# Kernel tuning notes

Hardware: AMD Instinct MI355X
Metric: run time of the kernel (lower is better)

## Reference

```python
import jax, jax.numpy as jnp
import numpy as np

EPS = 1e-12  # torch F.normalize eps

N, C, H, W = 64, 512, 40, 40
K = 64  # num_clusters


def setup_inputs() -> dict:
    key = jax.random.key(0)
    k1, k2, k3 = jax.random.split(key, 3)
    x = jax.random.normal(k1, (N, C, H, W), dtype=jnp.float32)
    conv_w = jax.random.normal(k2, (K, C, 1, 1), dtype=jnp.float32) * 0.05
    centroids = jax.random.uniform(k3, (K, C), dtype=jnp.float32)
    return {"x": x, "conv_w": conv_w, "centroids": centroids}


def _l2norm(v, axis):
    return v / jnp.maximum(jnp.sqrt(jnp.sum(v * v, axis=axis, keepdims=True)), EPS)


def reference(x, conv_w, centroids):
    n, c = x.shape[:2]
    k = conv_w.shape[0]
    # descriptor-wise L2 normalization over channels
    xn = _l2norm(x, axis=1)
    xf = xn.reshape(n, c, -1)  # [N, C, P]
    # 1x1 conv (no bias, vladv2=False) == per-pixel matmul with [K, C]
    logits = jnp.einsum('kc,ncp->nkp', conv_w.reshape(k, c), xf)
    a = jax.nn.softmax(logits, axis=1)  # soft assignment over clusters
    # VLAD: sum_p a[n,k,p] * (x[n,:,p] - centroid[k])  (weights are all-ones)
    vlad = jnp.einsum('nkp,ncp->nkc', a, xf) - a.sum(axis=-1)[:, :, None] * centroids[None]
    # intra-normalization over C, flatten, global L2 norm
    vlad = _l2norm(vlad, axis=2).reshape(n, -1)
    vlad = _l2norm(vlad, axis=1)
    return vlad
```

## Files before the change

kernel.cpp:

```cpp
#include <hip/hip_runtime.h>
#include <math.h>

#define EPSF 1e-12f


typedef short bf16x8 __attribute__((ext_vector_type(8)));
typedef float f32x4  __attribute__((ext_vector_type(4)));

__device__ __forceinline__ ushort f2b(float x) {
    unsigned u = __float_as_uint(x);
    return (ushort)((u + 0x7fffu + ((u >> 16) & 1u)) >> 16);
}

__global__ __launch_bounds__(256) void k0_wb(const float* __restrict__ W,
                                             ushort* __restrict__ Wb,
                                             float* __restrict__ asum) {
    int i = blockIdx.x * 256 + threadIdx.x;
    if (i < 64 * 512) Wb[i] = f2b(W[i]);
    if (i < 64 * 64) asum[i] = 0.f;
}

__global__ __launch_bounds__(256) void k2g_gemm1(const float* __restrict__ x,
                                                 const ushort* __restrict__ Wb,
                                                 ushort* __restrict__ a_t,
                                                 float* __restrict__ asum) {
    const int n = blockIdx.y;
    const int p0 = blockIdx.x * 64;
    const int wv = threadIdx.x >> 6, lane = threadIdx.x & 63;
    const int q = lane >> 4, l15 = lane & 15;
    const int pw = p0 + wv * 16;

    const float* xq = x + (size_t)n * 512 * 1600 + (size_t)q * 8 * 1600 + pw + l15;
    const ushort* brow = Wb + l15 * 512 + q * 8;

    f32x4 acc[4] = {};
    float ssp = 0.f;

    float fv[2][8];
    bf16x8 bwv[2][4];
    #pragma unroll
    for (int j = 0; j < 8; j++) fv[0][j] = xq[(size_t)j * 1600];
    #pragma unroll
    for (int nt = 0; nt < 4; nt++) bwv[0][nt] = *(const bf16x8*)(brow + nt * 16 * 512);

    #pragma unroll
    for (int kc = 0; kc < 16; kc++) {
        const int cur = kc & 1, nxt = cur ^ 1;
        if (kc < 15) {
            #pragma unroll
            for (int j = 0; j < 8; j++)
                fv[nxt][j] = xq[(size_t)((kc + 1) * 32 + j) * 1600];
            #pragma unroll
            for (int nt = 0; nt < 4; nt++)
                bwv[nxt][nt] = *(const bf16x8*)(brow + nt * 16 * 512 + (kc + 1) * 32);
        }
        bf16x8 af;
        #pragma unroll
        for (int j = 0; j < 8; j++) {
            float f = fv[cur][j];
            ssp = fmaf(f, f, ssp);
            af[j] = (short)f2b(f);
        }
        #pragma unroll
        for (int nt = 0; nt < 4; nt++)
            acc[nt] = __builtin_amdgcn_mfma_f32_16x16x32_bf16(af, bwv[cur][nt], acc[nt], 0, 0, 0);
    }

    ssp += __shfl_xor(ssp, 16, 64);
    ssp += __shfl_xor(ssp, 32, 64);
    float rn_l = 1.f / fmaxf(sqrtf(ssp), EPSF);
    float rnv[4];
    #pragma unroll
    for (int r = 0; r < 4; r++) rnv[r] = __shfl(rn_l, q * 4 + r, 64);

    float v[4][4];
    float mx[4] = {-3.4e38f, -3.4e38f, -3.4e38f, -3.4e38f};
    #pragma unroll
    for (int nt = 0; nt < 4; nt++)
        #pragma unroll
        for (int r = 0; r < 4; r++) {
            v[nt][r] = acc[nt][r] * rnv[r];
            mx[r] = fmaxf(mx[r], v[nt][r]);
        }
    #pragma unroll
    for (int s = 1; s <= 8; s <<= 1)
        #pragma unroll
        for (int r = 0; r < 4; r++) mx[r] = fmaxf(mx[r], __shfl_xor(mx[r], s, 64));
    float sm[4] = {0.f, 0.f, 0.f, 0.f};
    #pragma unroll
    for (int nt = 0; nt < 4; nt++)
        #pragma unroll
        for (int r = 0; r < 4; r++) { v[nt][r] = __expf(v[nt][r] - mx[r]); sm[r] += v[nt][r]; }
    #pragma unroll
    for (int s = 1; s <= 8; s <<= 1)
        #pragma unroll
        for (int r = 0; r < 4; r++) sm[r] += __shfl_xor(sm[r], s, 64);
    float inv[4];
    #pragma unroll
    for (int r = 0; r < 4; r++) inv[r] = 1.f / sm[r];
    #pragma unroll
    for (int nt = 0; nt < 4; nt++)
        #pragma unroll
        for (int r = 0; r < 4; r++) v[nt][r] *= inv[r];

    #pragma unroll
    for (int nt = 0; nt < 4; nt++) {
        float t = v[nt][0] + v[nt][1] + v[nt][2] + v[nt][3];
        t += __shfl_xor(t, 16, 64);
        t += __shfl_xor(t, 32, 64);
        if (lane < 16) atomicAdd(&asum[n * 64 + nt * 16 + lane], t);
    }

    __shared__ ushort abuf[4][64 * 24];
    #pragma unroll
    for (int nt = 0; nt < 4; nt++)
        #pragma unroll
        for (int r = 0; r < 4; r++)
            abuf[wv][(nt * 16 + l15) * 24 + q * 4 + r] = f2b(v[nt][r] * rnv[r]);
    __syncthreads();
    ushort* dst = a_t + ((size_t)n * 64 + lane) * 1600 + pw;
    const ushort* srcl = &abuf[wv][lane * 24];
    *(uint4*)(dst)     = *(const uint4*)(srcl);
    *(uint4*)(dst + 8) = *(const uint4*)(srcl + 8);
}

__global__ __launch_bounds__(512) void k3_gemm2(const ushort* __restrict__ a_t,
                                                const float* __restrict__ x,
                                                float* __restrict__ out) {
    const int n = blockIdx.y;
    const int c0 = blockIdx.x * 128;
    const int wv = threadIdx.x >> 6, lane = threadIdx.x & 63;
    const int q = lane >> 4, l15 = lane & 15;
    const int cw = c0 + wv * 16;

    const ushort* abase = a_t + ((size_t)n * 64 + l15) * 1600 + q * 8;
    const float*  xbase = x + ((size_t)n * 512 + cw + l15) * 1600 + q * 8;

    f32x4 acc[4] = {};
    #pragma unroll 2
    for (int pc = 0; pc < 1600; pc += 32) {
        bf16x8 af[4];
        #pragma unroll
        for (int mt = 0; mt < 4; mt++)
            af[mt] = *(const bf16x8*)(abase + (size_t)mt * 16 * 1600 + pc);
        const float* xr = xbase + pc;
        float4 f0 = *(const float4*)(xr);
        float4 f1 = *(const float4*)(xr + 4);
        bf16x8 b;
        b[0] = (short)f2b(f0.x); b[1] = (short)f2b(f0.y);
        b[2] = (short)f2b(f0.z); b[3] = (short)f2b(f0.w);
        b[4] = (short)f2b(f1.x); b[5] = (short)f2b(f1.y);
        b[6] = (short)f2b(f1.z); b[7] = (short)f2b(f1.w);
        #pragma unroll
        for (int mt = 0; mt < 4; mt++)
            acc[mt] = __builtin_amdgcn_mfma_f32_16x16x32_bf16(af[mt], b, acc[mt], 0, 0, 0);
    }
    float* ob = out + (size_t)n * 32768 + cw + l15;
    #pragma unroll
    for (int mt = 0; mt < 4; mt++)
        #pragma unroll
        for (int r = 0; r < 4; r++)
            ob[(mt * 16 + q * 4 + r) * 512] = acc[mt][r];
}

__global__ __launch_bounds__(512) void k4ab(const float* __restrict__ vraw,
                                            const float* __restrict__ asum,
                                            const float* __restrict__ cent,
                                            float* __restrict__ rn2,
                                            float* __restrict__ gn) {
    const int n = blockIdx.x;
    const int wv = threadIdx.x >> 6, lane = threadIdx.x & 63;
    __shared__ float rs[64];
    #pragma unroll
    for (int i = 0; i < 8; i++) {
        int k = wv * 8 + i;
        int row = n * 64 + k;
        const float4* vp = (const float4*)(vraw + (size_t)row * 512 + lane * 8);
        const float4* cp = (const float4*)(cent + k * 512 + lane * 8);
        float as = asum[row];
        float4 v0 = vp[0], v1 = vp[1], c0 = cp[0], c1 = cp[1];
        float s = 0.f, t;
        t = v0.x - as * c0.x; s = fmaf(t, t, s);
        t = v0.y - as * c0.y; s = fmaf(t, t, s);
        t = v0.z - as * c0.z; s = fmaf(t, t, s);
        t = v0.w - as * c0.w; s = fmaf(t, t, s);
        t = v1.x - as * c1.x; s = fmaf(t, t, s);
        t = v1.y - as * c1.y; s = fmaf(t, t, s);
        t = v1.z - as * c1.z; s = fmaf(t, t, s);
        t = v1.w - as * c1.w; s = fmaf(t, t, s);
        #pragma unroll
        for (int off = 32; off > 0; off >>= 1) s += __shfl_down(s, off, 64);
        if (lane == 0) { rs[k] = s; rn2[row] = s; }
    }
    __syncthreads();
    if (wv == 0) {
        float t = rs[lane];
        float d = fmaxf(sqrtf(t), EPSF);
        float r = t / (d * d);
        #pragma unroll
        for (int off = 32; off > 0; off >>= 1) r += __shfl_down(r, off, 64);
        if (lane == 0) gn[n] = fmaxf(sqrtf(r), EPSF);
    }
}

__global__ __launch_bounds__(256) void k4c_final(float* __restrict__ vout,
                                                 const float* __restrict__ asum,
                                                 const float* __restrict__ cent,
                                                 const float* __restrict__ rn2,
                                                 const float* __restrict__ gn) {
    int gid = blockIdx.x * 256 + threadIdx.x;
    int idx4 = gid * 4;
    int row = idx4 >> 9;
    int n = row >> 6, k = row & 63, c = idx4 & 511;
    float4 v  = *(const float4*)(vout + idx4);
    float4 cv = *(const float4*)(cent + k * 512 + c);
    float as = asum[row];
    float inv = 1.f / (fmaxf(sqrtf(rn2[row]), EPSF) * gn[n]);
    v.x = (v.x - as * cv.x) * inv;
    v.y = (v.y - as * cv.y) * inv;
    v.z = (v.z - as * cv.z) * inv;
    v.w = (v.w - as * cv.w) * inv;
    *(float4*)(vout + idx4) = v;
}

extern "C" void kernel_launch(void* const* d_in, const int* in_sizes, int n_in,
                              void* d_out, int out_size, void* d_ws, size_t ws_size,
                              hipStream_t stream) {
    const float* x    = (const float*)d_in[0];
    const float* W    = (const float*)d_in[1];
    const float* cent = (const float*)d_in[2];
    float* out = (float*)d_out;
    char* ws = (char*)d_ws;

    ushort* a_t  = (ushort*)(ws + 0);
    ushort* Wb   = (ushort*)(ws + 13107200);
    float*  asum = (float*)(ws + 13172736);
    float*  rn2  = (float*)(ws + 13189120);
    float*  gn   = (float*)(ws + 13205504);

    hipLaunchKernelGGL(k0_wb,     dim3(128),    dim3(256), 0, stream, W, Wb, asum);
    hipLaunchKernelGGL(k2g_gemm1, dim3(25, 64), dim3(256), 0, stream, x, Wb, a_t, asum);
    hipLaunchKernelGGL(k3_gemm2,  dim3(4, 64),  dim3(512), 0, stream, a_t, x, out);
    hipLaunchKernelGGL(k4ab,      dim3(64),     dim3(512), 0, stream, out, asum, cent, rn2, gn);
    hipLaunchKernelGGL(k4c_final, dim3(2048),   dim3(256), 0, stream, out, asum, cent, rn2, gn);
}
```

Before: 400.0 us.

## Fuse both GEMMs and softmax into one kernel with P-split partial sums

The logits GEMM, softmax and VLAD aggregation GEMM now run in one kernel. Each block streams its slice of pixels for one image, converts x to bf16 once, and keeps it in LDS for reuse by the second GEMM. This removes the second full read of x and the round trip of the assignment matrix through global memory. The pixel dimension is split into 5 chunks whose partial VLAD sums are written to workspace. A single finalize kernel then reduces the partials, subtracts the centroid term and applies both normalizations using an LDS stash, replacing two separate kernels. The cost is around 100KB of LDS per block, which limits occupancy, plus a partial-sum buffer that is written and read back by a finalize kernel with only 64 blocks.

```diff
diff --git a/kernel.cpp b/kernel.cpp
--- a/kernel.cpp
+++ b/kernel.cpp
@@ -20,177 +20,189 @@
     if (i < 64 * 64) asum[i] = 0.f;
 }
 
-__global__ __launch_bounds__(256) void k2g_gemm1(const float* __restrict__ x,
-                                                 const ushort* __restrict__ Wb,
-                                                 ushort* __restrict__ a_t,
-                                                 float* __restrict__ asum) {
-    const int n = blockIdx.y;
-    const int p0 = blockIdx.x * 64;
+__global__ __launch_bounds__(512, 2) void kf(const float* __restrict__ x,
+                                             const ushort* __restrict__ Wb,
+                                             float* __restrict__ part,
+                                             float* __restrict__ asum) {
+    const int cb = blockIdx.x;
+    const int n  = blockIdx.y;
     const int wv = threadIdx.x >> 6, lane = threadIdx.x & 63;
     const int q = lane >> 4, l15 = lane & 15;
-    const int pw = p0 + wv * 16;
-
-    const float* xq = x + (size_t)n * 512 * 1600 + (size_t)q * 8 * 1600 + pw + l15;
-    const ushort* brow = Wb + l15 * 512 + q * 8;
-
-    f32x4 acc[4] = {};
-    float ssp = 0.f;
-
-    float fv[2][8];
-    bf16x8 bwv[2][4];
-    #pragma unroll
-    for (int j = 0; j < 8; j++) fv[0][j] = xq[(size_t)j * 1600];
-    #pragma unroll
-    for (int nt = 0; nt < 4; nt++) bwv[0][nt] = *(const bf16x8*)(brow + nt * 16 * 512);
-
-    #pragma unroll
-    for (int kc = 0; kc < 16; kc++) {
-        const int cur = kc & 1, nxt = cur ^ 1;
-        if (kc < 15) {
-            #pragma unroll
-            for (int j = 0; j < 8; j++)
-                fv[nxt][j] = xq[(size_t)((kc + 1) * 32 + j) * 1600];
-            #pragma unroll
-            for (int nt = 0; nt < 4; nt++)
-                bwv[nxt][nt] = *(const bf16x8*)(brow + nt * 16 * 512 + (kc + 1) * 32);
-        }
-        bf16x8 af;
-        #pragma unroll
-        for (int j = 0; j < 8; j++) {
-            float f = fv[cur][j];
-            ssp = fmaf(f, f, ssp);
-            af[j] = (short)f2b(f);
-        }
-        #pragma unroll
-        for (int nt = 0; nt < 4; nt++)
-            acc[nt] = __builtin_amdgcn_mfma_f32_16x16x32_bf16(af, bwv[cur][nt], acc[nt], 0, 0, 0);
-    }
-
-    ssp += __shfl_xor(ssp, 16, 64);
-    ssp += __shfl_xor(ssp, 32, 64);
-    float rn_l = 1.f / fmaxf(sqrtf(ssp), EPSF);
-    float rnv[4];
-    #pragma unroll
-    for (int r = 0; r < 4; r++) rnv[r] = __shfl(rn_l, q * 4 + r, 64);
-
-    float v[4][4];
-    float mx[4] = {-3.4e38f, -3.4e38f, -3.4e38f, -3.4e38f};
-    #pragma unroll
-    for (int nt = 0; nt < 4; nt++)
-        #pragma unroll
-        for (int r = 0; r < 4; r++) {
-            v[nt][r] = acc[nt][r] * rnv[r];
-            mx[r] = fmaxf(mx[r], v[nt][r]);
-        }
-    #pragma unroll
-    for (int s = 1; s <= 8; s <<= 1)
-        #pragma unroll
-        for (int r = 0; r < 4; r++) mx[r] = fmaxf(mx[r], __shfl_xor(mx[r], s, 64));
-    float sm[4] = {0.f, 0.f, 0.f, 0.f};
-    #pragma unroll
-    for (int nt = 0; nt < 4; nt++)
-        #pragma unroll
-        for (int r = 0; r < 4; r++) { v[nt][r] = __expf(v[nt][r] - mx[r]); sm[r] += v[nt][r]; }
-    #pragma unroll
-    for (int s = 1; s <= 8; s <<= 1)
-        #pragma unroll
-        for (int r = 0; r < 4; r++) sm[r] += __shfl_xor(sm[r], s, 64);
-    float inv[4];
-    #pragma unroll
-    for (int r = 0; r < 4; r++) inv[r] = 1.f / sm[r];
-    #pragma unroll
-    for (int nt = 0; nt < 4; nt++)
-        #pragma unroll
-        for (int r = 0; r < 4; r++) v[nt][r] *= inv[r];
-
-    #pragma unroll
-    for (int nt = 0; nt < 4; nt++) {
-        float t = v[nt][0] + v[nt][1] + v[nt][2] + v[nt][3];
-        t += __shfl_xor(t, 16, 64);
-        t += __shfl_xor(t, 32, 64);
-        if (lane < 16) atomicAdd(&asum[n * 64 + nt * 16 + lane], t);
-    }
-
-    __shared__ ushort abuf[4][64 * 24];
-    #pragma unroll
-    for (int nt = 0; nt < 4; nt++)
-        #pragma unroll
-        for (int r = 0; r < 4; r++)
-            abuf[wv][(nt * 16 + l15) * 24 + q * 4 + r] = f2b(v[nt][r] * rnv[r]);
-    __syncthreads();
-    ushort* dst = a_t + ((size_t)n * 64 + lane) * 1600 + pw;
-    const ushort* srcl = &abuf[wv][lane * 24];
-    *(uint4*)(dst)     = *(const uint4*)(srcl);
-    *(uint4*)(dst + 8) = *(const uint4*)(srcl + 8);
-}
-
-__global__ __launch_bounds__(512) void k3_gemm2(const ushort* __restrict__ a_t,
-                                                const float* __restrict__ x,
-                                                float* __restrict__ out) {
-    const int n = blockIdx.y;
-    const int c0 = blockIdx.x * 128;
-    const int wv = threadIdx.x >> 6, lane = threadIdx.x & 63;
-    const int q = lane >> 4, l15 = lane & 15;
-    const int cw = c0 + wv * 16;
-
-    const ushort* abase = a_t + ((size_t)n * 64 + l15) * 1600 + q * 8;
-    const float*  xbase = x + ((size_t)n * 512 + cw + l15) * 1600 + q * 8;
-
-    f32x4 acc[4] = {};
-    #pragma unroll 2
-    for (int pc = 0; pc < 1600; pc += 32) {
-        bf16x8 af[4];
-        #pragma unroll
-        for (int mt = 0; mt < 4; mt++)
-            af[mt] = *(const bf16x8*)(abase + (size_t)mt * 16 * 1600 + pc);
-        const float* xr = xbase + pc;
-        float4 f0 = *(const float4*)(xr);
-        float4 f1 = *(const float4*)(xr + 4);
-        bf16x8 b;
-        b[0] = (short)f2b(f0.x); b[1] = (short)f2b(f0.y);
-        b[2] = (short)f2b(f0.z); b[3] = (short)f2b(f0.w);
-        b[4] = (short)f2b(f1.x); b[5] = (short)f2b(f1.y);
-        b[6] = (short)f2b(f1.z); b[7] = (short)f2b(f1.w);
-        #pragma unroll
-        for (int mt = 0; mt < 4; mt++)
-            acc[mt] = __builtin_amdgcn_mfma_f32_16x16x32_bf16(af[mt], b, acc[mt], 0, 0, 0);
-    }
-    float* ob = out + (size_t)n * 32768 + cw + l15;
+    const int pt = wv & 3, ch = wv >> 2;
+    const int cw = wv * 64;
+
+    __shared__ ushort xs[512 * 72];
+    __shared__ ushort abuf[64 * 72];
+    __shared__ float  accb[4 * 4 * 64 * 4];
+    __shared__ float  ssb[2 * 4 * 16];
+
+    f32x4 acc2[4][4] = {};
+
+    const ushort* wrow = Wb + l15 * 512 + ch * 256 + q * 8;
+
+    for (int s = 0; s < 5; s++) {
+        const float* xq = x + (size_t)n * 819200 + (size_t)(ch * 256 + q * 8) * 1600
+                            + (size_t)cb * 320 + s * 64 + pt * 16 + l15;
+        f32x4 acc1[4] = {};
+        float ssp = 0.f;
+        float fv[2][8];
+        #pragma unroll
+        for (int j = 0; j < 8; j++) fv[0][j] = xq[(size_t)j * 1600];
+        #pragma unroll
+        for (int kc = 0; kc < 8; kc++) {
+            const int cur = kc & 1, nxt = cur ^ 1;
+            if (kc < 7) {
+                #pragma unroll
+                for (int j = 0; j < 8; j++)
+                    fv[nxt][j] = xq[(size_t)((kc + 1) * 32 + j) * 1600];
+            }
+            bf16x8 af;
+            #pragma unroll
+            for (int j = 0; j < 8; j++) {
+                float f = fv[cur][j];
+                ssp = fmaf(f, f, ssp);
+                ushort b = f2b(f);
+                af[j] = (short)b;
+                xs[(ch * 256 + kc * 32 + q * 8 + j) * 72 + pt * 16 + l15] = b;
+            }
+            #pragma unroll
+            for (int nt = 0; nt < 4; nt++) {
+                bf16x8 bw = *(const bf16x8*)(wrow + nt * 16 * 512 + kc * 32);
+                acc1[nt] = __builtin_amdgcn_mfma_f32_16x16x32_bf16(af, bw, acc1[nt], 0, 0, 0);
+            }
+        }
+        ssp += __shfl_xor(ssp, 16, 64);
+        ssp += __shfl_xor(ssp, 32, 64);
+        if (lane < 16) ssb[ch * 64 + pt * 16 + lane] = ssp;
+        if (ch == 1) {
+            #pragma unroll
+            for (int nt = 0; nt < 4; nt++)
+                *(f32x4*)&accb[((pt * 4 + nt) * 64 + lane) * 4] = acc1[nt];
+        }
+        __syncthreads();
+
+        if (ch == 0) {
+            #pragma unroll
+            for (int nt = 0; nt < 4; nt++)
+                acc1[nt] += *(const f32x4*)&accb[((pt * 4 + nt) * 64 + lane) * 4];
+            float sst = ssb[pt * 16 + l15] + ssb[64 + pt * 16 + l15];
+            float rn_l = 1.f / fmaxf(sqrtf(sst), EPSF);
+            float rnv[4];
+            #pragma unroll
+            for (int r = 0; r < 4; r++) rnv[r] = __shfl(rn_l, q * 4 + r, 64);
+
+            float v[4][4];
+            float mx[4] = {-3.4e38f, -3.4e38f, -3.4e38f, -3.4e38f};
+            #pragma unroll
+            for (int nt = 0; nt < 4; nt++)
+                #pragma unroll
+                for (int r = 0; r < 4; r++) {
+                    v[nt][r] = acc1[nt][r] * rnv[r];
+                    mx[r] = fmaxf(mx[r], v[nt][r]);
+                }
+            #pragma unroll
+            for (int sh = 1; sh <= 8; sh <<= 1)
+                #pragma unroll
+                for (int r = 0; r < 4; r++) mx[r] = fmaxf(mx[r], __shfl_xor(mx[r], sh, 64));
+            float sm[4] = {0.f, 0.f, 0.f, 0.f};
+            #pragma unroll
+            for (int nt = 0; nt < 4; nt++)
+                #pragma unroll
+                for (int r = 0; r < 4; r++) { v[nt][r] = __expf(v[nt][r] - mx[r]); sm[r] += v[nt][r]; }
+            #pragma unroll
+            for (int sh = 1; sh <= 8; sh <<= 1)
+                #pragma unroll
+                for (int r = 0; r < 4; r++) sm[r] += __shfl_xor(sm[r], sh, 64);
+            float inv[4];
+            #pragma unroll
+            for (int r = 0; r < 4; r++) inv[r] = 1.f / sm[r];
+            #pragma unroll
+            for (int nt = 0; nt < 4; nt++)
+                #pragma unroll
+                for (int r = 0; r < 4; r++) v[nt][r] *= inv[r];
+
+            #pragma unroll
+            for (int nt = 0; nt < 4; nt++) {
+                float t = v[nt][0] + v[nt][1] + v[nt][2] + v[nt][3];
+                t += __shfl_xor(t, 16, 64);
+                t += __shfl_xor(t, 32, 64);
+                if (lane < 16) atomicAdd(&asum[n * 64 + nt * 16 + lane], t);
+            }
+
+            #pragma unroll
+            for (int nt = 0; nt < 4; nt++) {
+                ushort4 pk;
+                pk.x = f2b(v[nt][0] * rnv[0]);
+                pk.y = f2b(v[nt][1] * rnv[1]);
+                pk.z = f2b(v[nt][2] * rnv[2]);
+                pk.w = f2b(v[nt][3] * rnv[3]);
+                *(ushort4*)&abuf[(nt * 16 + l15) * 72 + pt * 16 + q * 4] = pk;
+            }
+        }
+        __syncthreads();
+
+        #pragma unroll
+        for (int ks = 0; ks < 2; ks++) {
+            bf16x8 av[4];
+            #pragma unroll
+            for (int mt = 0; mt < 4; mt++)
+                av[mt] = *(const bf16x8*)&abuf[(mt * 16 + l15) * 72 + ks * 32 + q * 8];
+            bf16x8 bv[4];
+            #pragma unroll
+            for (int nt = 0; nt < 4; nt++)
+                bv[nt] = *(const bf16x8*)&xs[(cw + nt * 16 + l15) * 72 + ks * 32 + q * 8];
+            #pragma unroll
+            for (int mt = 0; mt < 4; mt++)
+                #pragma unroll
+                for (int nt = 0; nt < 4; nt++)
+                    acc2[mt][nt] = __builtin_amdgcn_mfma_f32_16x16x32_bf16(av[mt], bv[nt], acc2[mt][nt], 0, 0, 0);
+        }
+        __syncthreads();
+    }
+
+    float* ob = part + ((size_t)cb * 64 + n) * 32768 + cw + l15;
     #pragma unroll
     for (int mt = 0; mt < 4; mt++)
         #pragma unroll
-        for (int r = 0; r < 4; r++)
-            ob[(mt * 16 + q * 4 + r) * 512] = acc[mt][r];
-}
-
-__global__ __launch_bounds__(512) void k4ab(const float* __restrict__ vraw,
-                                            const float* __restrict__ asum,
-                                            const float* __restrict__ cent,
-                                            float* __restrict__ rn2,
-                                            float* __restrict__ gn) {
+        for (int nt = 0; nt < 4; nt++)
+            #pragma unroll
+            for (int r = 0; r < 4; r++)
+                ob[(mt * 16 + q * 4 + r) * 512 + nt * 16] = acc2[mt][nt][r];
+}
+
+__global__ __launch_bounds__(512) void k4(const float* __restrict__ part,
+                                          const float* __restrict__ asum,
+                                          const float* __restrict__ cent,
+                                          float* __restrict__ out) {
     const int n = blockIdx.x;
     const int wv = threadIdx.x >> 6, lane = threadIdx.x & 63;
+    __shared__ float stash[64 * 512];
     __shared__ float rs[64];
+    __shared__ float gsh;
+
     #pragma unroll
     for (int i = 0; i < 8; i++) {
-        int k = wv * 8 + i;
-        int row = n * 64 + k;
-        const float4* vp = (const float4*)(vraw + (size_t)row * 512 + lane * 8);
-        const float4* cp = (const float4*)(cent + k * 512 + lane * 8);
-        float as = asum[row];
-        float4 v0 = vp[0], v1 = vp[1], c0 = cp[0], c1 = cp[1];
-        float s = 0.f, t;
-        t = v0.x - as * c0.x; s = fmaf(t, t, s);
-        t = v0.y - as * c0.y; s = fmaf(t, t, s);
-        t = v0.z - as * c0.z; s = fmaf(t, t, s);
-        t = v0.w - as * c0.w; s = fmaf(t, t, s);
-        t = v1.x - as * c1.x; s = fmaf(t, t, s);
-        t = v1.y - as * c1.y; s = fmaf(t, t, s);
-        t = v1.z - as * c1.z; s = fmaf(t, t, s);
-        t = v1.w - as * c1.w; s = fmaf(t, t, s);
+        const int k = wv * 8 + i;
+        const size_t ro = (size_t)n * 32768 + (size_t)k * 512 + lane * 8;
+        const float as = asum[n * 64 + k];
+        f32x4 a0 = {}, a1 = {};
+        #pragma unroll
+        for (int cbk = 0; cbk < 5; cbk++) {
+            const f32x4* pp = (const f32x4*)(part + (size_t)cbk * 2097152 + ro);
+            a0 += pp[0];
+            a1 += pp[1];
+        }
+        const f32x4* cp = (const f32x4*)(cent + k * 512 + lane * 8);
+        f32x4 v0 = a0 - cp[0] * as;
+        f32x4 v1 = a1 - cp[1] * as;
+        float s = 0.f;
+        #pragma unroll
+        for (int e = 0; e < 4; e++) { s = fmaf(v0[e], v0[e], s); s = fmaf(v1[e], v1[e], s); }
+        *(f32x4*)&stash[k * 512 + lane * 8] = v0;
+        *(f32x4*)&stash[k * 512 + lane * 8 + 4] = v1;
         #pragma unroll
         for (int off = 32; off > 0; off >>= 1) s += __shfl_down(s, off, 64);
-        if (lane == 0) { rs[k] = s; rn2[row] = s; }
+        if (lane == 0) rs[k] = s;
     }
     __syncthreads();
     if (wv == 0) {
@@ -199,28 +211,22 @@
         float r = t / (d * d);
         #pragma unroll
         for (int off = 32; off > 0; off >>= 1) r += __shfl_down(r, off, 64);
-        if (lane == 0) gn[n] = fmaxf(sqrtf(r), EPSF);
-    }
-}
-
-__global__ __launch_bounds__(256) void k4c_final(float* __restrict__ vout,
-                                                 const float* __restrict__ asum,
-                                                 const float* __restrict__ cent,
-                                                 const float* __restrict__ rn2,
-                                                 const float* __restrict__ gn) {
-    int gid = blockIdx.x * 256 + threadIdx.x;
-    int idx4 = gid * 4;
-    int row = idx4 >> 9;
-    int n = row >> 6, k = row & 63, c = idx4 & 511;
-    float4 v  = *(const float4*)(vout + idx4);
-    float4 cv = *(const float4*)(cent + k * 512 + c);
-    float as = asum[row];
-    float inv = 1.f / (fmaxf(sqrtf(rn2[row]), EPSF) * gn[n]);
-    v.x = (v.x - as * cv.x) * inv;
-    v.y = (v.y - as * cv.y) * inv;
-    v.z = (v.z - as * cv.z) * inv;
-    v.w = (v.w - as * cv.w) * inv;
-    *(float4*)(vout + idx4) = v;
+        if (lane == 0) gsh = fmaxf(sqrtf(r), EPSF);
+    }
+    __syncthreads();
+    const float g = gsh;
+    #pragma unroll
+    for (int i = 0; i < 8; i++) {
+        const int k = wv * 8 + i;
+        const float inv = 1.f / (fmaxf(sqrtf(rs[k]), EPSF) * g);
+        f32x4 v0 = *(const f32x4*)&stash[k * 512 + lane * 8];
+        f32x4 v1 = *(const f32x4*)&stash[k * 512 + lane * 8 + 4];
+        v0 *= inv;
+        v1 *= inv;
+        float* op = out + (size_t)n * 32768 + (size_t)k * 512 + lane * 8;
+        *(f32x4*)op = v0;
+        *(f32x4*)(op + 4) = v1;
+    }
 }
 
 extern "C" void kernel_launch(void* const* d_in, const int* in_sizes, int n_in,
@@ -232,15 +238,11 @@
     float* out = (float*)d_out;
     char* ws = (char*)d_ws;
 
-    ushort* a_t  = (ushort*)(ws + 0);
-    ushort* Wb   = (ushort*)(ws + 13107200);
-    float*  asum = (float*)(ws + 13172736);
-    float*  rn2  = (float*)(ws + 13189120);
-    float*  gn   = (float*)(ws + 13205504);
-
-    hipLaunchKernelGGL(k0_wb,     dim3(128),    dim3(256), 0, stream, W, Wb, asum);
-    hipLaunchKernelGGL(k2g_gemm1, dim3(25, 64), dim3(256), 0, stream, x, Wb, a_t, asum);
-    hipLaunchKernelGGL(k3_gemm2,  dim3(4, 64),  dim3(512), 0, stream, a_t, x, out);
-    hipLaunchKernelGGL(k4ab,      dim3(64),     dim3(512), 0, stream, out, asum, cent, rn2, gn);
-    hipLaunchKernelGGL(k4c_final, dim3(2048),   dim3(256), 0, stream, out, asum, cent, rn2, gn);
-}
+    float*  part = (float*)(ws + 0);
+    ushort* Wb   = (ushort*)(ws + 41943040);
+    float*  asum = (float*)(ws + 42008576);
+
+    hipLaunchKernelGGL(k0_wb, dim3(128),   dim3(256), 0, stream, W, Wb, asum);
+    hipLaunchKernelGGL(kf,    dim3(5, 64), dim3(512), 0, stream, x, Wb, part, asum);
+    hipLaunchKernelGGL(k4,    dim3(64),    dim3(512), 0, stream, part, asum, cent, out);
+}
```

After: 443.3 us. +10.8%, slower.

## Fuse VLAD normalization kernels and remap gemm2 blocks across XCDs

Applied to the files above, without the earlier changes.

The two-pass normalization (row norms plus global norm, then a separate elementwise rescale) becomes one kernel per batch item. It keeps the centroid-corrected rows in a 128 KB LDS stash and writes the final output directly. This drops one launch, one full re-read of the output and the rn2/gn scratch buffers, at the cost of large LDS use and occupancy of one block per CU. gemm2 also switches to a 1D grid with an XCD-aware index mapping, so the four channel tiles of the same batch item run on the same XCD and can share its assignment matrix in L2.

```diff
diff --git a/kernel.cpp b/kernel.cpp
--- a/kernel.cpp
+++ b/kernel.cpp
@@ -127,8 +127,11 @@
 __global__ __launch_bounds__(512) void k3_gemm2(const ushort* __restrict__ a_t,
                                                 const float* __restrict__ x,
                                                 float* __restrict__ out) {
-    const int n = blockIdx.y;
-    const int c0 = blockIdx.x * 128;
+    const int id = blockIdx.x;
+    const int xcd = id & 7, slot = id >> 3;
+    const int ct = slot & 3, ng = slot >> 2;
+    const int n = ng * 8 + xcd;
+    const int c0 = ct * 128;
     const int wv = threadIdx.x >> 6, lane = threadIdx.x & 63;
     const int q = lane >> 4, l15 = lane & 15;
     const int cw = c0 + wv * 16;
@@ -163,34 +166,34 @@
             ob[(mt * 16 + q * 4 + r) * 512] = acc[mt][r];
 }
 
-__global__ __launch_bounds__(512) void k4ab(const float* __restrict__ vraw,
-                                            const float* __restrict__ asum,
-                                            const float* __restrict__ cent,
-                                            float* __restrict__ rn2,
-                                            float* __restrict__ gn) {
+__global__ __launch_bounds__(512) void k4(const float* __restrict__ vraw,
+                                          const float* __restrict__ asum,
+                                          const float* __restrict__ cent,
+                                          float* __restrict__ out) {
     const int n = blockIdx.x;
     const int wv = threadIdx.x >> 6, lane = threadIdx.x & 63;
+    __shared__ float stash[64 * 512];
     __shared__ float rs[64];
+    __shared__ float gsh;
+
     #pragma unroll
     for (int i = 0; i < 8; i++) {
-        int k = wv * 8 + i;
-        int row = n * 64 + k;
-        const float4* vp = (const float4*)(vraw + (size_t)row * 512 + lane * 8);
-        const float4* cp = (const float4*)(cent + k * 512 + lane * 8);
-        float as = asum[row];
-        float4 v0 = vp[0], v1 = vp[1], c0 = cp[0], c1 = cp[1];
-        float s = 0.f, t;
-        t = v0.x - as * c0.x; s = fmaf(t, t, s);
-        t = v0.y - as * c0.y; s = fmaf(t, t, s);
-        t = v0.z - as * c0.z; s = fmaf(t, t, s);
-        t = v0.w - as * c0.w; s = fmaf(t, t, s);
-        t = v1.x - as * c1.x; s = fmaf(t, t, s);
-        t = v1.y - as * c1.y; s = fmaf(t, t, s);
-        t = v1.z - as * c1.z; s = fmaf(t, t, s);
-        t = v1.w - as * c1.w; s = fmaf(t, t, s);
+        const int k = wv * 8 + i;
+        const size_t ro = (size_t)n * 32768 + (size_t)k * 512 + lane * 8;
+        const float as = asum[n * 64 + k];
+        const f32x4* pp = (const f32x4*)(vraw + ro);
+        f32x4 a0 = pp[0], a1 = pp[1];
+        const f32x4* cp = (const f32x4*)(cent + k * 512 + lane * 8);
+        f32x4 v0 = a0 - cp[0] * as;
+        f32x4 v1 = a1 - cp[1] * as;
+        float s = 0.f;
+        #pragma unroll
+        for (int e = 0; e < 4; e++) { s = fmaf(v0[e], v0[e], s); s = fmaf(v1[e], v1[e], s); }
+        *(f32x4*)&stash[k * 512 + lane * 8] = v0;
+        *(f32x4*)&stash[k * 512 + lane * 8 + 4] = v1;
         #pragma unroll
         for (int off = 32; off > 0; off >>= 1) s += __shfl_down(s, off, 64);
-        if (lane == 0) { rs[k] = s; rn2[row] = s; }
+        if (lane == 0) rs[k] = s;
     }
     __syncthreads();
     if (wv == 0) {
@@ -199,28 +202,22 @@
         float r = t / (d * d);
         #pragma unroll
         for (int off = 32; off > 0; off >>= 1) r += __shfl_down(r, off, 64);
-        if (lane == 0) gn[n] = fmaxf(sqrtf(r), EPSF);
-    }
-}
-
-__global__ __launch_bounds__(256) void k4c_final(float* __restrict__ vout,
-                                                 const float* __restrict__ asum,
-                                                 const float* __restrict__ cent,
-                                                 const float* __restrict__ rn2,
-                                                 const float* __restrict__ gn) {
-    int gid = blockIdx.x * 256 + threadIdx.x;
-    int idx4 = gid * 4;
-    int row = idx4 >> 9;
-    int n = row >> 6, k = row & 63, c = idx4 & 511;
-    float4 v  = *(const float4*)(vout + idx4);
-    float4 cv = *(const float4*)(cent + k * 512 + c);
-    float as = asum[row];
-    float inv = 1.f / (fmaxf(sqrtf(rn2[row]), EPSF) * gn[n]);
-    v.x = (v.x - as * cv.x) * inv;
-    v.y = (v.y - as * cv.y) * inv;
-    v.z = (v.z - as * cv.z) * inv;
-    v.w = (v.w - as * cv.w) * inv;
-    *(float4*)(vout + idx4) = v;
+        if (lane == 0) gsh = fmaxf(sqrtf(r), EPSF);
+    }
+    __syncthreads();
+    const float g = gsh;
+    #pragma unroll
+    for (int i = 0; i < 8; i++) {
+        const int k = wv * 8 + i;
+        const float inv = 1.f / (fmaxf(sqrtf(rs[k]), EPSF) * g);
+        f32x4 v0 = *(const f32x4*)&stash[k * 512 + lane * 8];
+        f32x4 v1 = *(const f32x4*)&stash[k * 512 + lane * 8 + 4];
+        v0 *= inv;
+        v1 *= inv;
+        float* op = out + (size_t)n * 32768 + (size_t)k * 512 + lane * 8;
+        *(f32x4*)op = v0;
+        *(f32x4*)(op + 4) = v1;
+    }
 }
 
 extern "C" void kernel_launch(void* const* d_in, const int* in_sizes, int n_in,
@@ -235,12 +232,9 @@
     ushort* a_t  = (ushort*)(ws + 0);
     ushort* Wb   = (ushort*)(ws + 13107200);
     float*  asum = (float*)(ws + 13172736);
-    float*  rn2  = (float*)(ws + 13189120);
-    float*  gn   = (float*)(ws + 13205504);
 
     hipLaunchKernelGGL(k0_wb,     dim3(128),    dim3(256), 0, stream, W, Wb, asum);
     hipLaunchKernelGGL(k2g_gemm1, dim3(25, 64), dim3(256), 0, stream, x, Wb, a_t, asum);
-    hipLaunchKernelGGL(k3_gemm2,  dim3(4, 64),  dim3(512), 0, stream, a_t, x, out);
-    hipLaunchKernelGGL(k4ab,      dim3(64),     dim3(512), 0, stream, out, asum, cent, rn2, gn);
-    hipLaunchKernelGGL(k4c_final, dim3(2048),   dim3(256), 0, stream, out, asum, cent, rn2, gn);
-}
+    hipLaunchKernelGGL(k3_gemm2,  dim3(256),    dim3(512), 0, stream, a_t, x, out);
+    hipLaunchKernelGGL(k4,        dim3(64),     dim3(512), 0, stream, out, asum, cent, out);
+}
```

New measurement: 397.6 us. No clear change (-0.6%).
